# Kernel optimization log

Hardware: AMD Instinct MI355X
Metric: run time of the kernel (lower is better)

The kernel has to match this reference:

```python
import jax, jax.numpy as jnp
import numpy as np

B, S, D, H = 2, 2048, 2048, 16
DPH = D // H  # 128


def setup_inputs() -> dict:
    key = jax.random.key(0)
    k1, _ = jax.random.split(key)
    query = jax.random.normal(k1, (B, S, D), dtype=jnp.float32)
    mask = jnp.ones((B, S), dtype=jnp.int32)  # True = allow attention
    return {"query": query, "mask": mask}


def reference(query, mask):
    # Faithful to the given snippet: q_lin/k_lin/v_lin/out_lin are defined in
    # __init__ but never invoked in forward, and attn_mask is constructed but
    # never applied to dot_prod. Self-attention path: key = value = query.
    b, q_len, dim = query.shape
    scale = np.sqrt(DPH).astype(np.float32)

    # prepare_head: [B, S, D] -> [B, H, S, dph]
    q = query.reshape(b, q_len, H, DPH).transpose(0, 2, 1, 3) / scale
    k = query.reshape(b, q_len, H, DPH).transpose(0, 2, 1, 3)
    v = k

    # dot_prod = (q/scale) @ k^T : [B, H, Sq, Sk]
    dot_prod = jnp.einsum('bhqd,bhkd->bhqk', q, k)

    # fp32 softmax, cast back to query dtype (mask is NOT applied in source)
    attn_weights = jax.nn.softmax(dot_prod.astype(jnp.float32), axis=-1).astype(query.dtype)

    attentioned = jnp.einsum('bhqk,bhkd->bhqd', attn_weights, v)
    out = attentioned.transpose(0, 2, 1, 3).reshape(b, q_len, dim)

    # new_incr_state tensors (prev_key/prev_value in [B, H, S, dph], prev_mask)
    prev_key = k.reshape(b, H, q_len, DPH)
    prev_value = v.reshape(b, H, q_len, DPH)
    # dot_prod returned as [B*H, Sq, Sk] to match source shape
    return out, prev_key, prev_value, mask, dot_prod.reshape(b * H, q_len, q_len)
```

## Files before the change

### kernel.cpp

```cpp
#include <hip/hip_runtime.h>
#include <hip/hip_bf16.h>

#define BB 2
#define HH 16
#define SS 2048
#define DD 2048
#define DPH_ 128
#define QBLK 128
#define KBLK 64
#define NT (SS / KBLK)

#define KSTR 136
#define VSTR 72
#define PSTR 72

typedef __bf16 bf16x8 __attribute__((ext_vector_type(8)));
typedef unsigned short u16x8 __attribute__((ext_vector_type(8)));
typedef float f32x4 __attribute__((ext_vector_type(4)));

__device__ __forceinline__ unsigned short f2bfbits(float f) {
  unsigned u = __builtin_bit_cast(unsigned, f);
  u += 0x7FFFu + ((u >> 16) & 1u);
  return (unsigned short)(u >> 16);
}
__device__ __forceinline__ __bf16 f2bf(float f) {
  unsigned short s = f2bfbits(f);
  return __builtin_bit_cast(__bf16, s);
}
__device__ __forceinline__ void nt_store4(const float4& v, float* p) {
  f32x4 t = {v.x, v.y, v.z, v.w};
  __builtin_nontemporal_store(t, (f32x4*)p);
}

template <bool PRE>
__global__ __launch_bounds__(256)
void preproc(const float* __restrict__ q, const int* __restrict__ mask,
             __bf16* __restrict__ qb, float* __restrict__ pk,
             float* __restrict__ pv, float* __restrict__ omask) {
  const size_t i = (size_t)blockIdx.x * 256 + threadIdx.x;
  const size_t e = i * 8;
  const size_t d = e & (DD - 1);
  const size_t s = (e >> 11) & (SS - 1);
  const size_t b = e >> 22;
  const float4 v0 = *(const float4*)(q + e);
  const float4 v1 = *(const float4*)(q + e + 4);
  const size_t h = d >> 7, dph = d & 127;
  float* po = pk + ((b * HH + h) * SS + s) * DPH_ + dph;
  float* vo = pv + ((b * HH + h) * SS + s) * DPH_ + dph;
  nt_store4(v0, po);
  nt_store4(v1, po + 4);
  nt_store4(v0, vo);
  nt_store4(v1, vo + 4);
  if constexpr (PRE) {
    u16x8 t;
    t[0] = f2bfbits(v0.x); t[1] = f2bfbits(v0.y);
    t[2] = f2bfbits(v0.z); t[3] = f2bfbits(v0.w);
    t[4] = f2bfbits(v1.x); t[5] = f2bfbits(v1.y);
    t[6] = f2bfbits(v1.z); t[7] = f2bfbits(v1.w);
    *(u16x8*)(qb + e) = t;
  }
  if (i < (size_t)BB * SS) omask[i] = (float)mask[i];
}

template <bool PRE>
__global__ __launch_bounds__(512, 4)
void attn_fused(const __bf16* __restrict__ qb, const float* __restrict__ qf,
                float* __restrict__ out, float* __restrict__ dot) {
  __shared__ __bf16 kls[KBLK * KSTR];
  __shared__ __bf16 vls[DPH_ * VSTR];
  __shared__ __bf16 pls[8 * 16 * PSTR];

  const int bid = blockIdx.x;
  const int xcd = bid & 7;
  const int t_  = bid >> 3;
  const int qt  = t_ & 15;
  const int G   = (t_ >> 4) * 8 + xcd;
  const int h   = G & 15;
  const int b   = G >> 4;

  const int tid  = threadIdx.x;
  const int wid  = tid >> 6;
  const int lane = tid & 63;
  const int g    = lane >> 4;
  const int c    = lane & 15;
  const int skv  = lane;

  const int qbase = qt * QBLK;
  const float scale = 0.08838834764831845f;

  const size_t headoff = (size_t)b * SS * DD + (size_t)h * DPH_;
  const __bf16* qbh = PRE ? qb + headoff : nullptr;
  const float*  qfh = qf + headoff;

  bf16x8 aq[4];
  {
    const int row = qbase + wid * 16 + c;
    if constexpr (PRE) {
      const __bf16* p = qbh + (size_t)row * DD + 8 * g;
      #pragma unroll
      for (int st = 0; st < 4; ++st) aq[st] = *(const bf16x8*)(p + st * 32);
    } else {
      const float* p = qfh + (size_t)row * DD + 8 * g;
      #pragma unroll
      for (int st = 0; st < 4; ++st) {
        u16x8 t;
        #pragma unroll
        for (int i2 = 0; i2 < 8; ++i2) t[i2] = f2bfbits(p[st * 32 + i2]);
        aq[st] = __builtin_bit_cast(bf16x8, t);
      }
    }
  }

  auto load_tile = [&](int kvb, bf16x8& a0, bf16x8& a1) {
    if constexpr (PRE) {
      const __bf16* p = qbh + (size_t)(kvb + skv) * DD + wid * 8;
      a0 = *(const bf16x8*)p;
      a1 = *(const bf16x8*)(p + 64);
    } else {
      const float* p = qfh + (size_t)(kvb + skv) * DD + wid * 8;
      const float4 f0 = *(const float4*)p;
      const float4 f1 = *(const float4*)(p + 4);
      const float4 f2 = *(const float4*)(p + 64);
      const float4 f3 = *(const float4*)(p + 68);
      u16x8 t0, t1;
      t0[0] = f2bfbits(f0.x); t0[1] = f2bfbits(f0.y);
      t0[2] = f2bfbits(f0.z); t0[3] = f2bfbits(f0.w);
      t0[4] = f2bfbits(f1.x); t0[5] = f2bfbits(f1.y);
      t0[6] = f2bfbits(f1.z); t0[7] = f2bfbits(f1.w);
      t1[0] = f2bfbits(f2.x); t1[1] = f2bfbits(f2.y);
      t1[2] = f2bfbits(f2.z); t1[3] = f2bfbits(f2.w);
      t1[4] = f2bfbits(f3.x); t1[5] = f2bfbits(f3.y);
      t1[6] = f2bfbits(f3.z); t1[7] = f2bfbits(f3.w);
      a0 = __builtin_bit_cast(bf16x8, t0);
      a1 = __builtin_bit_cast(bf16x8, t1);
    }
  };
  auto write_tile = [&](bf16x8 a0, bf16x8 a1) {
    *(bf16x8*)(&kls[skv * KSTR + wid * 8]) = a0;
    *(bf16x8*)(&kls[skv * KSTR + (wid + 8) * 8]) = a1;
    #pragma unroll
    for (int j = 0; j < 8; ++j) {
      vls[(wid * 8 + j) * VSTR + skv] = a0[j];
      vls[((wid + 8) * 8 + j) * VSTR + skv] = a1[j];
    }
  };

  const f32x4 zero4 = {0.f, 0.f, 0.f, 0.f};
  f32x4 o[8];
  #pragma unroll
  for (int t = 0; t < 8; ++t) o[t] = zero4;
  float m[4], l[4];
  #pragma unroll
  for (int r = 0; r < 4; ++r) { m[r] = -1e30f; l[r] = 0.0f; }

  float* __restrict__ dotb = dot + ((size_t)(b * HH + h) << 22);

  bf16x8 p0, p1;
  load_tile(0, p0, p1);
  write_tile(p0, p1);
  __syncthreads();

  for (int kt = 0; kt < NT; ++kt) {
    const int kvbase = kt * KBLK;

    f32x4 s[4];
    #pragma unroll
    for (int ct = 0; ct < 4; ++ct) s[ct] = zero4;
    #pragma unroll
    for (int st = 0; st < 4; ++st) {
      #pragma unroll
      for (int ct = 0; ct < 4; ++ct) {
        bf16x8 bk = *(const bf16x8*)(&kls[(ct * 16 + c) * KSTR + st * 32 + 8 * g]);
        s[ct] = __builtin_amdgcn_mfma_f32_16x16x32_bf16(aq[st], bk, s[ct], 0, 0, 0);
      }
    }

    if (kt + 1 < NT) load_tile(kvbase + KBLK, p0, p1);

    #pragma unroll
    for (int ct = 0; ct < 4; ++ct) s[ct] *= scale;
    #pragma unroll
    for (int r = 0; r < 4; ++r) {
      float* dp = dotb + (size_t)(qbase + wid * 16 + 4 * g + r) * SS + kvbase + c;
      #pragma unroll
      for (int ct = 0; ct < 4; ++ct)
        __builtin_nontemporal_store(s[ct][r], dp + ct * 16);
    }

    float alpha[4];
    #pragma unroll
    for (int r = 0; r < 4; ++r) {
      float tm = fmaxf(fmaxf(s[0][r], s[1][r]), fmaxf(s[2][r], s[3][r]));
      #pragma unroll
      for (int off = 1; off < 16; off <<= 1) tm = fmaxf(tm, __shfl_xor(tm, off));
      float mn = fmaxf(m[r], tm);
      alpha[r] = __expf(m[r] - mn);
      m[r] = mn;
    }
    float rs[4] = {0.f, 0.f, 0.f, 0.f};
    #pragma unroll
    for (int ct = 0; ct < 4; ++ct) {
      #pragma unroll
      for (int r = 0; r < 4; ++r) {
        float p = __expf(s[ct][r] - m[r]);
        s[ct][r] = p;
        rs[r] += p;
      }
    }
    #pragma unroll
    for (int r = 0; r < 4; ++r) {
      #pragma unroll
      for (int off = 1; off < 16; off <<= 1) rs[r] += __shfl_xor(rs[r], off);
      l[r] = l[r] * alpha[r] + rs[r];
      #pragma unroll
      for (int t = 0; t < 8; ++t) o[t][r] *= alpha[r];
    }

    {
      __bf16* pw = &pls[wid * 16 * PSTR];
      #pragma unroll
      for (int ct = 0; ct < 4; ++ct)
        #pragma unroll
        for (int r = 0; r < 4; ++r)
          pw[(4 * g + r) * PSTR + ct * 16 + c] = f2bf(s[ct][r]);
    }

    #pragma unroll
    for (int kk = 0; kk < 2; ++kk) {
      bf16x8 ap = *(const bf16x8*)(&pls[(wid * 16 + c) * PSTR + kk * 32 + 8 * g]);
      #pragma unroll
      for (int t = 0; t < 8; ++t) {
        bf16x8 bv = *(const bf16x8*)(&vls[(t * 16 + c) * VSTR + kk * 32 + 8 * g]);
        o[t] = __builtin_amdgcn_mfma_f32_16x16x32_bf16(ap, bv, o[t], 0, 0, 0);
      }
    }

    __syncthreads();
    if (kt + 1 < NT) write_tile(p0, p1);
    __syncthreads();
  }

  #pragma unroll
  for (int r = 0; r < 4; ++r) {
    float inv = 1.0f / l[r];
    float* op = out + (size_t)(b * SS + qbase + wid * 16 + 4 * g + r) * DD + h * DPH_ + c;
    #pragma unroll
    for (int t = 0; t < 8; ++t)
      __builtin_nontemporal_store(o[t][r] * inv, op + t * 16);
  }
}

extern "C" void kernel_launch(void* const* d_in, const int* in_sizes, int n_in,
                              void* d_out, int out_size, void* d_ws, size_t ws_size,
                              hipStream_t stream) {
  const float* q    = (const float*)d_in[0];
  const int*   mask = (const int*)d_in[1];
  float* out = (float*)d_out;

  float* o_out  = out;
  float* o_pk   = out + 8388608;
  float* o_pv   = out + 16777216;
  float* o_mask = out + 25165824;
  float* o_dot  = out + 25169920;

  const size_t need = (size_t)BB * SS * DD * sizeof(__bf16);
  const dim3 agrid(512);

  if (ws_size >= need) {
    __bf16* qbf = (__bf16*)d_ws;
    preproc<true><<<4096, 256, 0, stream>>>(q, mask, qbf, o_pk, o_pv, o_mask);
    attn_fused<true><<<agrid, 512, 0, stream>>>(qbf, q, o_out, o_dot);
  } else {
    preproc<false><<<4096, 256, 0, stream>>>(q, mask, nullptr, o_pk, o_pv, o_mask);
    attn_fused<false><<<agrid, 512, 0, stream>>>(nullptr, q, o_out, o_dot);
  }
}
```

Baseline: 207.0 us.

## Move prev_key/prev_value copies into attention epilogue and raise MFMA wave priority

Writing the prev_key/prev_value head-transposed copies now happens at the end of the attention kernel instead of in the preprocessing kernel. Each attention block copies its own 128-row query tile for its head. The preprocessing kernel then only converts to bf16 and writes the mask, so it carries less store traffic. s_setprio is also raised around the two MFMA loops so matrix work gets issue priority over softmax and memory work from other waves. The copies now sit on the attention kernel's tail, which may lengthen it, and the fp32 input is re-read there.

Measured after the change: 195.1 us, median of 3. 5.7% less time.

```diff
diff --git a/kernel.cpp b/kernel.cpp
--- a/kernel.cpp
+++ b/kernel.cpp
@@ -35,23 +35,12 @@
 template <bool PRE>
 __global__ __launch_bounds__(256)
 void preproc(const float* __restrict__ q, const int* __restrict__ mask,
-             __bf16* __restrict__ qb, float* __restrict__ pk,
-             float* __restrict__ pv, float* __restrict__ omask) {
+             __bf16* __restrict__ qb, float* __restrict__ omask) {
   const size_t i = (size_t)blockIdx.x * 256 + threadIdx.x;
   const size_t e = i * 8;
-  const size_t d = e & (DD - 1);
-  const size_t s = (e >> 11) & (SS - 1);
-  const size_t b = e >> 22;
-  const float4 v0 = *(const float4*)(q + e);
-  const float4 v1 = *(const float4*)(q + e + 4);
-  const size_t h = d >> 7, dph = d & 127;
-  float* po = pk + ((b * HH + h) * SS + s) * DPH_ + dph;
-  float* vo = pv + ((b * HH + h) * SS + s) * DPH_ + dph;
-  nt_store4(v0, po);
-  nt_store4(v1, po + 4);
-  nt_store4(v0, vo);
-  nt_store4(v1, vo + 4);
   if constexpr (PRE) {
+    const float4 v0 = *(const float4*)(q + e);
+    const float4 v1 = *(const float4*)(q + e + 4);
     u16x8 t;
     t[0] = f2bfbits(v0.x); t[1] = f2bfbits(v0.y);
     t[2] = f2bfbits(v0.z); t[3] = f2bfbits(v0.w);
@@ -65,7 +54,8 @@
 template <bool PRE>
 __global__ __launch_bounds__(512, 4)
 void attn_fused(const __bf16* __restrict__ qb, const float* __restrict__ qf,
-                float* __restrict__ out, float* __restrict__ dot) {
+                float* __restrict__ out, float* __restrict__ dot,
+                float* __restrict__ pk, float* __restrict__ pv) {
   __shared__ __bf16 kls[KBLK * KSTR];
   __shared__ __bf16 vls[DPH_ * VSTR];
   __shared__ __bf16 pls[8 * 16 * PSTR];
@@ -166,6 +156,7 @@
     f32x4 s[4];
     #pragma unroll
     for (int ct = 0; ct < 4; ++ct) s[ct] = zero4;
+    __builtin_amdgcn_s_setprio(1);
     #pragma unroll
     for (int st = 0; st < 4; ++st) {
       #pragma unroll
@@ -174,6 +165,7 @@
         s[ct] = __builtin_amdgcn_mfma_f32_16x16x32_bf16(aq[st], bk, s[ct], 0, 0, 0);
       }
     }
+    __builtin_amdgcn_s_setprio(0);
 
     if (kt + 1 < NT) load_tile(kvbase + KBLK, p0, p1);
 
@@ -225,6 +217,7 @@
           pw[(4 * g + r) * PSTR + ct * 16 + c] = f2bf(s[ct][r]);
     }
 
+    __builtin_amdgcn_s_setprio(1);
     #pragma unroll
     for (int kk = 0; kk < 2; ++kk) {
       bf16x8 ap = *(const bf16x8*)(&pls[(wid * 16 + c) * PSTR + kk * 32 + 8 * g]);
@@ -234,6 +227,7 @@
         o[t] = __builtin_amdgcn_mfma_f32_16x16x32_bf16(ap, bv, o[t], 0, 0, 0);
       }
     }
+    __builtin_amdgcn_s_setprio(0);
 
     __syncthreads();
     if (kt + 1 < NT) write_tile(p0, p1);
@@ -247,6 +241,18 @@
     #pragma unroll
     for (int t = 0; t < 8; ++t)
       __builtin_nontemporal_store(o[t][r] * inv, op + t * 16);
+  }
+
+  {
+    const size_t bh = (size_t)b * HH + h;
+    const int col = (tid & 31) * 4;
+    #pragma unroll
+    for (int rr = 0; rr < QBLK; rr += 16) {
+      const int row = qbase + rr + (tid >> 5);
+      const float4 v = *(const float4*)(qfh + (size_t)row * DD + col);
+      nt_store4(v, pk + (bh * SS + row) * DPH_ + col);
+      nt_store4(v, pv + (bh * SS + row) * DPH_ + col);
+    }
   }
 }
 
@@ -268,10 +274,10 @@
 
   if (ws_size >= need) {
     __bf16* qbf = (__bf16*)d_ws;
-    preproc<true><<<4096, 256, 0, stream>>>(q, mask, qbf, o_pk, o_pv, o_mask);
-    attn_fused<true><<<agrid, 512, 0, stream>>>(qbf, q, o_out, o_dot);
+    preproc<true><<<4096, 256, 0, stream>>>(q, mask, qbf, o_mask);
+    attn_fused<true><<<agrid, 512, 0, stream>>>(qbf, q, o_out, o_dot, o_pk, o_pv);
   } else {
-    preproc<false><<<4096, 256, 0, stream>>>(q, mask, nullptr, o_pk, o_pv, o_mask);
-    attn_fused<false><<<agrid, 512, 0, stream>>>(nullptr, q, o_out, o_dot);
-  }
-}
+    preproc<false><<<4096, 256, 0, stream>>>(q, mask, nullptr, o_mask);
+    attn_fused<false><<<agrid, 512, 0, stream>>>(nullptr, q, o_out, o_dot, o_pk, o_pv);
+  }
+}
```
